# Performance work log

Hardware: AMD Instinct MI355X
Metric: run time of the kernel (lower is better)

## Reference

```python
import jax, jax.numpy as jnp
import numpy as np

LEAK = 0.9
BASE_THRESH = 1.0
BN_EPS = 1e-5

@jax.custom_vjp
def spike_fn(x):
    return (x >= 0).astype(x.dtype)

def _spike_fwd(x):
    return (x >= 0).astype(x.dtype), x

def _spike_bwd(x, g):
    return (g / (1.0 + 5.0 * jnp.abs(x)) ** 2,)

spike_fn.defvjp(_spike_fwd, _spike_bwd)


def setup_inputs() -> dict:
    key = jax.random.key(0)
    ks = jax.random.split(key, 8)
    B, T, C, H, NC, DT = 256, 2048, 64, 64, 4, 50
    kin_spikes_seq = jax.random.normal(ks[0], (B, T, C), dtype=jnp.float32)
    tda_features = jax.random.normal(ks[1], (B, DT), dtype=jnp.float32)
    # spatial_conv1x1: Linear(64 -> 64, bias=False); weight [out, in]
    W_spatial = jax.random.normal(ks[2], (H, C), dtype=jnp.float32) / np.sqrt(C)
    bn_gamma = jnp.ones((H,), dtype=jnp.float32)
    bn_beta = jnp.zeros((H,), dtype=jnp.float32)
    # class_conv1x1: Linear(64 -> 4, bias=False)
    W_class = jax.random.normal(ks[3], (NC, H), dtype=jnp.float32) / np.sqrt(H)
    lateral = jnp.eye(NC, dtype=jnp.float32) * 0.8 - 0.1
    # tda_to_thresh: Linear(50 -> 4)
    W_tda = jax.random.normal(ks[4], (NC, DT), dtype=jnp.float32) / np.sqrt(DT)
    b_tda = jnp.zeros((NC,), dtype=jnp.float32)
    return {
        "kin_spikes_seq": kin_spikes_seq,
        "tda_features": tda_features,
        "W_spatial": W_spatial,
        "bn_gamma": bn_gamma,
        "bn_beta": bn_beta,
        "W_class": W_class,
        "lateral": lateral,
        "W_tda": W_tda,
        "b_tda": b_tda,
    }


def reference(kin_spikes_seq, tda_features, W_spatial, bn_gamma, bn_beta,
              W_class, lateral, W_tda, b_tda):
    # [B, T, C] @ [C, H] -> [B, T, H]
    x_proj = jnp.einsum("btc,hc->bth", kin_spikes_seq, W_spatial)
    # BatchNorm1d in training mode: per-channel stats over (B, T)
    mean = jnp.mean(x_proj, axis=(0, 1))
    var = jnp.var(x_proj, axis=(0, 1))
    x_proj = (x_proj - mean) * jax.lax.rsqrt(var + BN_EPS) * bn_gamma + bn_beta

    tda_mod = jax.nn.sigmoid(tda_features @ W_tda.T + b_tda) * 0.5  # [B, 4]
    dynamic_thresh = BASE_THRESH + tda_mod

    B = kin_spikes_seq.shape[0]
    H, NC = W_class.shape[1], W_class.shape[0]
    mem1 = jnp.zeros((B, H), dtype=x_proj.dtype)
    mem2 = jnp.zeros((B, NC), dtype=x_proj.dtype)
    spike_sum = jnp.zeros((B, NC), dtype=x_proj.dtype)

    def step(carry, xt):
        mem1, mem2, ssum = carry
        mem1 = LEAK * mem1 + xt
        spk1 = spike_fn(mem1 - BASE_THRESH)
        mem1 = mem1 * (1.0 - spk1)
        cur2 = (spk1 @ W_class.T) @ lateral  # [B, 4]
        mem2 = LEAK * mem2 + cur2
        spk2 = spike_fn(mem2 - dynamic_thresh)
        mem2 = mem2 * (1.0 - spk2)
        return (mem1, mem2, ssum + spk2), None

    xs = jnp.swapaxes(x_proj, 0, 1)  # [T, B, H]
    (mem1, mem2, spike_sum), _ = jax.lax.scan(step, (mem1, mem2, spike_sum), xs)
    return spike_sum
```

## Files before the change

kernel.cpp:

```cpp
#include <hip/hip_runtime.h>
#include <cstdint>
#include <cstddef>
#include <cmath>

#define BB 256
#define TB 2048
#define NROWS (BB*TB)
#define R1 256
#define NBLK_K1 (NROWS/R1)
#define NBLK1 4096

typedef float f32x4 __attribute__((ext_vector_type(4)));
typedef float f32x2 __attribute__((ext_vector_type(2)));

#define OFF_X      0ull
#define SZ_X       ((size_t)NROWS*64*4)
#define OFF_PART   (OFF_X + SZ_X)
#define SZ_PART    ((size_t)128*NBLK1*4)
#define OFF_STAT   (OFF_PART + SZ_PART)
#define SZ_STAT    (128*8)

__global__ __launch_bounds__(256, 2) void k1_gemm(const float* __restrict__ kin,
                                                  const float* __restrict__ Wsp,
                                                  float* __restrict__ xproj,
                                                  float* __restrict__ partials) {
  __shared__ float4 As[R1 * 16];
  __shared__ f32x4 Wp[32 * 32];
  const int tid = threadIdx.x;
  const int ty = tid >> 3;
  const int tx = tid & 7;
  const size_t r0 = (size_t)blockIdx.x * R1;

  const f32x4* kin4 = (const f32x4*)(kin + r0 * 64);
  #pragma unroll
  for (int k = 0; k < 16; ++k) {
    int idx = k * 256 + tid;
    int r = idx >> 4, cc = idx & 15;
    f32x4 v = __builtin_nontemporal_load(&kin4[idx]);
    As[r * 16 + (cc ^ ((r >> 3) & 7))] = make_float4(v.x, v.y, v.z, v.w);
  }
  #pragma unroll
  for (int k = 0; k < 4; ++k) {
    int idx = k * 256 + tid;
    int p = idx >> 5, q = idx & 31;
    float2 w0 = *(const float2*)(Wsp + (2 * p) * 64 + 2 * q);
    float2 w1 = *(const float2*)(Wsp + (2 * p + 1) * 64 + 2 * q);
    Wp[p * 32 + (q ^ ((p >> 2) & 7))] = (f32x4){w0.x, w1.x, w0.y, w1.y};
  }
  __syncthreads();

  f32x2 acc2[8][4];
  #pragma unroll
  for (int i = 0; i < 8; ++i)
    #pragma unroll
    for (int jp = 0; jp < 4; ++jp) acc2[i][jp] = (f32x2){0.f, 0.f};

  #pragma unroll 1
  for (int cc = 0; cc < 16; ++cc) {
    float4 av[8];
    f32x4 q0[4], q1[4];
    #pragma unroll
    for (int i = 0; i < 8; ++i)
      av[i] = As[(8 * ty + i) * 16 + (cc ^ (ty & 7))];
    #pragma unroll
    for (int jp = 0; jp < 4; ++jp) {
      const int p = 4 * tx + jp;
      q0[jp] = Wp[p * 32 + ((2 * cc)     ^ tx)];
      q1[jp] = Wp[p * 32 + ((2 * cc + 1) ^ tx)];
    }
    #pragma unroll
    for (int i = 0; i < 8; ++i) {
      #pragma unroll
      for (int jp = 0; jp < 4; ++jp) {
        acc2[i][jp] = __builtin_elementwise_fma((f32x2){av[i].x, av[i].x}, q0[jp].xy, acc2[i][jp]);
        acc2[i][jp] = __builtin_elementwise_fma((f32x2){av[i].y, av[i].y}, q0[jp].zw, acc2[i][jp]);
        acc2[i][jp] = __builtin_elementwise_fma((f32x2){av[i].z, av[i].z}, q1[jp].xy, acc2[i][jp]);
        acc2[i][jp] = __builtin_elementwise_fma((f32x2){av[i].w, av[i].w}, q1[jp].zw, acc2[i][jp]);
      }
    }
  }

  #pragma unroll
  for (int i = 0; i < 8; ++i) {
    const size_t row = r0 + 8 * ty + i;
    f32x4 lo = {acc2[i][0].x, acc2[i][0].y, acc2[i][1].x, acc2[i][1].y};
    f32x4 hi = {acc2[i][2].x, acc2[i][2].y, acc2[i][3].x, acc2[i][3].y};
    *(f32x4*)(xproj + row * 64 + 8 * tx)     = lo;
    *(f32x4*)(xproj + row * 64 + 8 * tx + 4) = hi;
  }

  __syncthreads();
  float* Sm = (float*)As;
  float* Sq = Sm + 64 * 33;
  #pragma unroll
  for (int j = 0; j < 8; ++j) {
    const int col = 8 * tx + j;
    float s = 0.f, q = 0.f;
    #pragma unroll
    for (int i = 0; i < 8; ++i) {
      float v = (j & 1) ? acc2[i][j >> 1].y : acc2[i][j >> 1].x;
      s += v;
      q += v * v;
    }
    Sm[col * 33 + ty] = s;
    Sq[col * 33 + ty] = q;
  }
  __syncthreads();
  if (tid < 64) {
    float s0 = 0.f, q0 = 0.f, s1 = 0.f, q1 = 0.f;
    #pragma unroll
    for (int g = 0; g < 16; ++g)  { s0 += Sm[tid * 33 + g]; q0 += Sq[tid * 33 + g]; }
    #pragma unroll
    for (int g = 16; g < 32; ++g) { s1 += Sm[tid * 33 + g]; q1 += Sq[tid * 33 + g]; }
    const size_t p0 = 2 * (size_t)blockIdx.x;
    partials[(size_t)tid * NBLK1 + p0]            = s0;
    partials[(size_t)tid * NBLK1 + p0 + 1]        = s1;
    partials[(size_t)(64 + tid) * NBLK1 + p0]     = q0;
    partials[(size_t)(64 + tid) * NBLK1 + p0 + 1] = q1;
  }
}

__global__ __launch_bounds__(256) void k2a_reduce(const float* __restrict__ partials,
                                                  double* __restrict__ statd) {
  __shared__ double sd[256];
  const int idx = blockIdx.x;
  double acc = 0.0;
  for (int k = threadIdx.x; k < NBLK1; k += 256)
    acc += (double)partials[(size_t)idx * NBLK1 + k];
  sd[threadIdx.x] = acc;
  __syncthreads();
  for (int s = 128; s > 0; s >>= 1) {
    if (threadIdx.x < s) sd[threadIdx.x] += sd[threadIdx.x + s];
    __syncthreads();
  }
  if (threadIdx.x == 0) statd[idx] = sd[0];
}

#define K45_LOAD(BUF, TBASE)                                             \
  { _Pragma("unroll") for (int k_ = 0; k_ < 16; ++k_) {                  \
      f32x4 v = *(const f32x4*)(cr + (TBASE) + 4 * k_);                  \
      BUF[4 * k_] = v.x; BUF[4 * k_ + 1] = v.y;                          \
      BUF[4 * k_ + 2] = v.z; BUF[4 * k_ + 3] = v.w; } }

#define K45_CHUNK(CUR, NXT0)                                  \
  { _Pragma("unroll") for (int i_ = 0; i_ < 64; ++i_) {       \
      bool sp = (mem2 >= th);                                 \
      cnt += sp ? 1u : 0u;                                    \
      float xn = (i_ < 63) ? CUR[(i_ + 1) & 63] : (NXT0);     \
      mem2 = sp ? xn : fmaf(mem2, 0.9f, xn);                  \
    } }

#define PROD_WRITE(BF)                                                        \
  { _Pragma("unroll") for (int h2 = 0; h2 < 64; ++h2) {                       \
      float pv;                                                               \
      switch (h2 & 3) {                                                       \
        case 0: pv = pregs[h2 >> 2].x; break;                                 \
        case 1: pv = pregs[h2 >> 2].y; break;                                 \
        case 2: pv = pregs[h2 >> 2].z; break;                                 \
        default: pv = pregs[h2 >> 2].w; break;                                \
      }                                                                       \
      xs[BF][h2][4 * ((lane >> 2) ^ (h2 & 7)) + (lane & 3)] = pv;             \
    } }

#define PROD_ISSUE(C)                                                         \
  { const f32x4* xr_ = (const f32x4*)(xproj + ((size_t)b * TB +               \
                                      (size_t)(C) * 64 + lane) * 64);         \
    _Pragma("unroll") for (int k_ = 0; k_ < 16; ++k_) pregs[k_] = xr_[k_]; }

__global__ __launch_bounds__(256) void k345_scan(const float* __restrict__ xproj,
                                                 const double* __restrict__ statd,
                                                 const float* __restrict__ gamma,
                                                 const float* __restrict__ beta,
                                                 const float* __restrict__ Wc,
                                                 const float* __restrict__ lat,
                                                 const float* __restrict__ tda,
                                                 const float* __restrict__ Wtda,
                                                 const float* __restrict__ btda,
                                                 float* __restrict__ out) {
  __shared__ float xs[4][64][64];
  __shared__ unsigned long long masksL[TB];
  __shared__ float WcL[256];
  __shared__ float latL[16];
  __shared__ float thL[4];
  __shared__ float lbuf[4][TB + 4];
  const int tid = threadIdx.x, b = blockIdx.x;
  const int lane = tid & 63;
  const int wv = tid >> 6;

  WcL[tid] = Wc[tid];
  if (tid < 16) latL[tid] = lat[tid];

  float sc = 0.f, sh = 0.f, mem = 0.f;
  f32x4 pregs[16];

  if (wv == 1 || wv == 2) {
    const int c = wv - 1;
    PROD_ISSUE(c)
    PROD_WRITE(c)
  } else if (wv == 3) {
    if (lane < 4) {
      const int j = lane;
      double acc = (double)btda[j];
      for (int k = 0; k < 50; ++k)
        acc += (double)tda[b * 50 + k] * (double)Wtda[j * 50 + k];
      double sig = 1.0 / (1.0 + exp(-acc));
      thL[j] = (float)(1.0 + 0.5 * sig);
    }
  } else {
    const int h = lane;
    const double mean = statd[h] / (double)NROWS;
    const double ex2  = statd[64 + h] / (double)NROWS;
    const double var  = ex2 - mean * mean;
    const double scd  = (double)gamma[h] / sqrt(var + 1e-5);
    sc = (float)scd;
    sh = (float)((double)beta[h] - mean * scd);
  }
  __syncthreads();

  if (wv == 3) { PROD_ISSUE(2) }
  else if (wv == 1) { PROD_ISSUE(3) }
  else if (wv == 0) {
    mem = fmaf(xs[0][lane][4 * (lane & 7)], sc, sh);
  }

  #pragma unroll 1
  for (int n = 0; n < 32; ++n) {
    if (n + 2 < 32 && wv == 1 + ((n + 2) % 3)) {
      const int bf = (n + 2) & 3;
      PROD_WRITE(bf)
    }
    if (n + 4 < 32 && wv == 1 + ((n + 1) % 3)) {
      PROD_ISSUE(n + 4)
    }
    if (wv == 0) {
      const int bf = n & 3, swz = lane & 7;
      const float4* xrow = (const float4*)&xs[bf][lane][0];
      float4 v4[16];
      #pragma unroll
      for (int i = 0; i < 16; ++i) v4[i] = xrow[i ^ swz];
      float vv[64];
      #pragma unroll
      for (int i = 0; i < 16; ++i) {
        vv[4*i] = v4[i].x; vv[4*i+1] = v4[i].y; vv[4*i+2] = v4[i].z; vv[4*i+3] = v4[i].w;
      }
      const float nxt0 = (n < 31) ? xs[(n + 1) & 3][lane][4 * swz] : 0.f;
      unsigned long long keep = 0ull;
      #pragma unroll
      for (int i_ = 0; i_ < 64; ++i_) {
        bool sp = (mem >= 1.0f);
        unsigned long long mb = __ballot(sp);
        if (lane == i_) keep = mb;
        float xrn = (i_ < 63) ? vv[(i_ + 1) & 63] : nxt0;
        float xn = fmaf(xrn, sc, sh);
        mem = sp ? xn : fmaf(mem, 0.9f, xn);
      }
      masksL[n * 64 + lane] = keep;
    }
    asm volatile("s_waitcnt lgkmcnt(0)" ::: "memory");
    __builtin_amdgcn_sched_barrier(0);
    __builtin_amdgcn_s_barrier();
  }
  __syncthreads();

  #pragma unroll 1
  for (int c = 0; c < 8; ++c) {
    const int t = c * 256 + tid;
    const unsigned long long m = masksL[t];
    const unsigned lo = (unsigned)m, hi = (unsigned)(m >> 32);
    float v0 = 0.f, v1 = 0.f, v2 = 0.f, v3 = 0.f;
    #pragma unroll
    for (int hh = 0; hh < 32; ++hh) {
      const float bit = (float)((lo >> hh) & 1u);
      v0 = fmaf(bit, WcL[hh],       v0);
      v1 = fmaf(bit, WcL[64 + hh],  v1);
      v2 = fmaf(bit, WcL[128 + hh], v2);
      v3 = fmaf(bit, WcL[192 + hh], v3);
    }
    #pragma unroll
    for (int hh = 32; hh < 64; ++hh) {
      const float bit = (float)((hi >> (hh - 32)) & 1u);
      v0 = fmaf(bit, WcL[hh],       v0);
      v1 = fmaf(bit, WcL[64 + hh],  v1);
      v2 = fmaf(bit, WcL[128 + hh], v2);
      v3 = fmaf(bit, WcL[192 + hh], v3);
    }
    { float cx = v0 * latL[0];  cx = fmaf(v1, latL[4],  cx); cx = fmaf(v2, latL[8],  cx); cx = fmaf(v3, latL[12], cx); lbuf[0][t] = cx; }
    { float cx = v0 * latL[1];  cx = fmaf(v1, latL[5],  cx); cx = fmaf(v2, latL[9],  cx); cx = fmaf(v3, latL[13], cx); lbuf[1][t] = cx; }
    { float cx = v0 * latL[2];  cx = fmaf(v1, latL[6],  cx); cx = fmaf(v2, latL[10], cx); cx = fmaf(v3, latL[14], cx); lbuf[2][t] = cx; }
    { float cx = v0 * latL[3];  cx = fmaf(v1, latL[7],  cx); cx = fmaf(v2, latL[11], cx); cx = fmaf(v3, latL[15], cx); lbuf[3][t] = cx; }
  }
  __syncthreads();
  if (tid >= 64) return;

  const int j4 = tid & 3;
  const float th = thL[j4];
  const float* cr = lbuf[j4];
  float ca[64], cb[64];

  K45_LOAD(ca, 0)
  float mem2 = ca[0];
  unsigned cnt = 0;

  #pragma unroll 1
  for (int t0 = 0; t0 < TB; t0 += 128) {
    K45_LOAD(cb, t0 + 64)
    K45_CHUNK(ca, cb[0])
    if (t0 + 128 < TB) { K45_LOAD(ca, t0 + 128) }
    K45_CHUNK(cb, ca[0])
  }
  if (tid < 4) out[b * 4 + j4] = (float)cnt;
}

extern "C" void kernel_launch(void* const* d_in, const int* in_sizes, int n_in,
                              void* d_out, int out_size, void* d_ws, size_t ws_size,
                              hipStream_t stream) {
  const float* kin   = (const float*)d_in[0];
  const float* tda   = (const float*)d_in[1];
  const float* Wsp   = (const float*)d_in[2];
  const float* gamma = (const float*)d_in[3];
  const float* beta  = (const float*)d_in[4];
  const float* Wc    = (const float*)d_in[5];
  const float* lat   = (const float*)d_in[6];
  const float* Wtda  = (const float*)d_in[7];
  const float* btda  = (const float*)d_in[8];

  char* ws = (char*)d_ws;
  float*  xproj    = (float*)(ws + OFF_X);
  float*  partials = (float*)(ws + OFF_PART);
  double* statd    = (double*)(ws + OFF_STAT);
  float*  out      = (float*)d_out;

  k1_gemm  <<<dim3(NBLK_K1), dim3(256), 0, stream>>>(kin, Wsp, xproj, partials);
  k2a_reduce<<<dim3(128),  dim3(256), 0, stream>>>(partials, statd);
  k345_scan<<<dim3(BB),    dim3(256), 0, stream>>>(xproj, statd, gamma, beta,
                                                   Wc, lat, tda, Wtda, btda, out);
}
```

Baseline: 150.7 us.

## Stream GEMM A operand from global into registers with double buffering

New measurement: 562.5 us. 273% more time.

```diff
diff --git a/kernel.cpp b/kernel.cpp
--- a/kernel.cpp
+++ b/kernel.cpp
@@ -20,25 +20,18 @@
 #define OFF_STAT   (OFF_PART + SZ_PART)
 #define SZ_STAT    (128*8)
 
-__global__ __launch_bounds__(256, 2) void k1_gemm(const float* __restrict__ kin,
+__global__ __launch_bounds__(256, 3) void k1_gemm(const float* __restrict__ kin,
                                                   const float* __restrict__ Wsp,
                                                   float* __restrict__ xproj,
                                                   float* __restrict__ partials) {
-  __shared__ float4 As[R1 * 16];
   __shared__ f32x4 Wp[32 * 32];
+  __shared__ float Sm[64 * 33];
+  __shared__ float Sq[64 * 33];
   const int tid = threadIdx.x;
   const int ty = tid >> 3;
   const int tx = tid & 7;
   const size_t r0 = (size_t)blockIdx.x * R1;
 
-  const f32x4* kin4 = (const f32x4*)(kin + r0 * 64);
-  #pragma unroll
-  for (int k = 0; k < 16; ++k) {
-    int idx = k * 256 + tid;
-    int r = idx >> 4, cc = idx & 15;
-    f32x4 v = __builtin_nontemporal_load(&kin4[idx]);
-    As[r * 16 + (cc ^ ((r >> 3) & 7))] = make_float4(v.x, v.y, v.z, v.w);
-  }
   #pragma unroll
   for (int k = 0; k < 4; ++k) {
     int idx = k * 256 + tid;
@@ -49,6 +42,12 @@
   }
   __syncthreads();
 
+  const float* abase = kin + (r0 + 8 * (size_t)ty) * 64;
+  f32x4 av[2][8];
+  #pragma unroll
+  for (int i = 0; i < 8; ++i)
+    av[0][i] = *(const f32x4*)(abase + i * 64);
+
   f32x2 acc2[8][4];
   #pragma unroll
   for (int i = 0; i < 8; ++i)
@@ -57,11 +56,13 @@
 
   #pragma unroll 1
   for (int cc = 0; cc < 16; ++cc) {
-    float4 av[8];
+    const int buf = cc & 1;
+    if (cc < 15) {
+      #pragma unroll
+      for (int i = 0; i < 8; ++i)
+        av[buf ^ 1][i] = *(const f32x4*)(abase + i * 64 + (cc + 1) * 4);
+    }
     f32x4 q0[4], q1[4];
-    #pragma unroll
-    for (int i = 0; i < 8; ++i)
-      av[i] = As[(8 * ty + i) * 16 + (cc ^ (ty & 7))];
     #pragma unroll
     for (int jp = 0; jp < 4; ++jp) {
       const int p = 4 * tx + jp;
@@ -70,12 +71,13 @@
     }
     #pragma unroll
     for (int i = 0; i < 8; ++i) {
+      f32x4 a = av[buf][i];
       #pragma unroll
       for (int jp = 0; jp < 4; ++jp) {
-        acc2[i][jp] = __builtin_elementwise_fma((f32x2){av[i].x, av[i].x}, q0[jp].xy, acc2[i][jp]);
-        acc2[i][jp] = __builtin_elementwise_fma((f32x2){av[i].y, av[i].y}, q0[jp].zw, acc2[i][jp]);
-        acc2[i][jp] = __builtin_elementwise_fma((f32x2){av[i].z, av[i].z}, q1[jp].xy, acc2[i][jp]);
-        acc2[i][jp] = __builtin_elementwise_fma((f32x2){av[i].w, av[i].w}, q1[jp].zw, acc2[i][jp]);
+        acc2[i][jp] = __builtin_elementwise_fma((f32x2){a.x, a.x}, q0[jp].xy, acc2[i][jp]);
+        acc2[i][jp] = __builtin_elementwise_fma((f32x2){a.y, a.y}, q0[jp].zw, acc2[i][jp]);
+        acc2[i][jp] = __builtin_elementwise_fma((f32x2){a.z, a.z}, q1[jp].xy, acc2[i][jp]);
+        acc2[i][jp] = __builtin_elementwise_fma((f32x2){a.w, a.w}, q1[jp].zw, acc2[i][jp]);
       }
     }
   }
@@ -89,9 +91,6 @@
     *(f32x4*)(xproj + row * 64 + 8 * tx + 4) = hi;
   }
 
-  __syncthreads();
-  float* Sm = (float*)As;
-  float* Sq = Sm + 64 * 33;
   #pragma unroll
   for (int j = 0; j < 8; ++j) {
     const int col = 8 * tx + j;
```

## Stream scan input via global_load_lds in the scan wave, drop producer waves and barriers

Applied to the files above, without the earlier changes.

Result: slower. 178.3 us (+18.3%).

```diff
diff --git a/kernel.cpp b/kernel.cpp
--- a/kernel.cpp
+++ b/kernel.cpp
@@ -19,6 +19,12 @@
 #define SZ_PART    ((size_t)128*NBLK1*4)
 #define OFF_STAT   (OFF_PART + SZ_PART)
 #define SZ_STAT    (128*8)
+
+__device__ __forceinline__ void gll16(const float* g, void* l) {
+  __builtin_amdgcn_global_load_lds(
+      (const __attribute__((address_space(1))) unsigned int*)g,
+      (__attribute__((address_space(3))) unsigned int*)l, 16, 0, 0);
+}
 
 __global__ __launch_bounds__(256, 2) void k1_gemm(const float* __restrict__ kin,
                                                   const float* __restrict__ Wsp,
@@ -150,22 +156,11 @@
       mem2 = sp ? xn : fmaf(mem2, 0.9f, xn);                  \
     } }
 
-#define PROD_WRITE(BF)                                                        \
-  { _Pragma("unroll") for (int h2 = 0; h2 < 64; ++h2) {                       \
-      float pv;                                                               \
-      switch (h2 & 3) {                                                       \
-        case 0: pv = pregs[h2 >> 2].x; break;                                 \
-        case 1: pv = pregs[h2 >> 2].y; break;                                 \
-        case 2: pv = pregs[h2 >> 2].z; break;                                 \
-        default: pv = pregs[h2 >> 2].w; break;                                \
-      }                                                                       \
-      xs[BF][h2][4 * ((lane >> 2) ^ (h2 & 7)) + (lane & 3)] = pv;             \
+#define ISSUE_CHUNK(BF, C)                                                   \
+  { const float* gb_ = xproj + ((size_t)b * TB + (size_t)(C) * 64) * 64;     \
+    _Pragma("unroll") for (int k_ = 0; k_ < 16; ++k_) {                      \
+      gll16(gb_ + k_ * 256 + lane * 4, &xs[BF][4 * k_][0]);                  \
     } }
-
-#define PROD_ISSUE(C)                                                         \
-  { const f32x4* xr_ = (const f32x4*)(xproj + ((size_t)b * TB +               \
-                                      (size_t)(C) * 64 + lane) * 64);         \
-    _Pragma("unroll") for (int k_ = 0; k_ < 16; ++k_) pregs[k_] = xr_[k_]; }
 
 __global__ __launch_bounds__(256) void k345_scan(const float* __restrict__ xproj,
                                                  const double* __restrict__ statd,
@@ -190,13 +185,55 @@
   WcL[tid] = Wc[tid];
   if (tid < 16) latL[tid] = lat[tid];
 
-  float sc = 0.f, sh = 0.f, mem = 0.f;
-  f32x4 pregs[16];
-
-  if (wv == 1 || wv == 2) {
-    const int c = wv - 1;
-    PROD_ISSUE(c)
-    PROD_WRITE(c)
+  if (wv == 0) {
+    const int h = lane;
+    const double mean = statd[h] / (double)NROWS;
+    const double ex2  = statd[64 + h] / (double)NROWS;
+    const double var  = ex2 - mean * mean;
+    const double scd  = (double)gamma[h] / sqrt(var + 1e-5);
+    const float sc = (float)scd;
+    const float sh = (float)((double)beta[h] - mean * scd);
+
+    asm volatile("s_waitcnt vmcnt(0)" ::: "memory");
+    ISSUE_CHUNK(0, 0)
+    ISSUE_CHUNK(1, 1)
+
+    float mem = 0.f;
+    #pragma unroll 1
+    for (int n = 0; n < 32; ++n) {
+      const int bf = n & 3;
+      if (n + 2 < 32) {
+        ISSUE_CHUNK((n + 2) & 3, n + 2)
+        asm volatile("s_waitcnt vmcnt(32)" ::: "memory");
+      } else if (n == 30) {
+        asm volatile("s_waitcnt vmcnt(16)" ::: "memory");
+      } else {
+        asm volatile("s_waitcnt vmcnt(0)" ::: "memory");
+      }
+      if (n == 0) mem = fmaf(xs[0][0][lane], sc, sh);
+
+      unsigned long long keep = 0ull;
+      #pragma unroll
+      for (int i_ = 0; i_ < 63; ++i_) {
+        bool sp = (mem >= 1.0f);
+        unsigned long long mb = __ballot(sp);
+        if (lane == i_) keep = mb;
+        float xrn = xs[bf][i_ + 1][lane];
+        float xn = fmaf(xrn, sc, sh);
+        mem = sp ? xn : fmaf(mem, 0.9f, xn);
+      }
+      if (n <= 29) { asm volatile("s_waitcnt vmcnt(16)" ::: "memory"); }
+      else if (n == 30) { asm volatile("s_waitcnt vmcnt(0)" ::: "memory"); }
+      {
+        bool sp = (mem >= 1.0f);
+        unsigned long long mb = __ballot(sp);
+        if (lane == 63) keep = mb;
+        float xrn = (n < 31) ? xs[(n + 1) & 3][0][lane] : 0.f;
+        float xn = fmaf(xrn, sc, sh);
+        mem = sp ? xn : fmaf(mem, 0.9f, xn);
+      }
+      masksL[n * 64 + lane] = keep;
+    }
   } else if (wv == 3) {
     if (lane < 4) {
       const int j = lane;
@@ -206,59 +243,6 @@
       double sig = 1.0 / (1.0 + exp(-acc));
       thL[j] = (float)(1.0 + 0.5 * sig);
     }
-  } else {
-    const int h = lane;
-    const double mean = statd[h] / (double)NROWS;
-    const double ex2  = statd[64 + h] / (double)NROWS;
-    const double var  = ex2 - mean * mean;
-    const double scd  = (double)gamma[h] / sqrt(var + 1e-5);
-    sc = (float)scd;
-    sh = (float)((double)beta[h] - mean * scd);
-  }
-  __syncthreads();
-
-  if (wv == 3) { PROD_ISSUE(2) }
-  else if (wv == 1) { PROD_ISSUE(3) }
-  else if (wv == 0) {
-    mem = fmaf(xs[0][lane][4 * (lane & 7)], sc, sh);
-  }
-
-  #pragma unroll 1
-  for (int n = 0; n < 32; ++n) {
-    if (n + 2 < 32 && wv == 1 + ((n + 2) % 3)) {
-      const int bf = (n + 2) & 3;
-      PROD_WRITE(bf)
-    }
-    if (n + 4 < 32 && wv == 1 + ((n + 1) % 3)) {
-      PROD_ISSUE(n + 4)
-    }
-    if (wv == 0) {
-      const int bf = n & 3, swz = lane & 7;
-      const float4* xrow = (const float4*)&xs[bf][lane][0];
-      float4 v4[16];
-      #pragma unroll
-      for (int i = 0; i < 16; ++i) v4[i] = xrow[i ^ swz];
-      float vv[64];
-      #pragma unroll
-      for (int i = 0; i < 16; ++i) {
-        vv[4*i] = v4[i].x; vv[4*i+1] = v4[i].y; vv[4*i+2] = v4[i].z; vv[4*i+3] = v4[i].w;
-      }
-      const float nxt0 = (n < 31) ? xs[(n + 1) & 3][lane][4 * swz] : 0.f;
-      unsigned long long keep = 0ull;
-      #pragma unroll
-      for (int i_ = 0; i_ < 64; ++i_) {
-        bool sp = (mem >= 1.0f);
-        unsigned long long mb = __ballot(sp);
-        if (lane == i_) keep = mb;
-        float xrn = (i_ < 63) ? vv[(i_ + 1) & 63] : nxt0;
-        float xn = fmaf(xrn, sc, sh);
-        mem = sp ? xn : fmaf(mem, 0.9f, xn);
-      }
-      masksL[n * 64 + lane] = keep;
-    }
-    asm volatile("s_waitcnt lgkmcnt(0)" ::: "memory");
-    __builtin_amdgcn_sched_barrier(0);
-    __builtin_amdgcn_s_barrier();
   }
   __syncthreads();
 
```
